# Kernel optimization log

Hardware: AMD Instinct MI355X
Metric: run time of the kernel (lower is better)

## Reference

```python
import jax, jax.numpy as jnp
import numpy as np

NUM_HEADS = 16
NEG = -1e9


def setup_inputs() -> dict:
    key = jax.random.key(0)
    ks = jax.random.split(key, 9)
    B, S, D = 1, 4096, 1024
    s = 1.0 / np.sqrt(D)
    return {
        "x": jax.random.normal(ks[0], (B, S, D), dtype=jnp.float32),
        "wq": jax.random.normal(ks[1], (D, D), dtype=jnp.float32) * s,
        "bq": jax.random.normal(ks[2], (D,), dtype=jnp.float32) * s,
        "wk": jax.random.normal(ks[3], (D, D), dtype=jnp.float32) * s,
        "bk": jax.random.normal(ks[4], (D,), dtype=jnp.float32) * s,
        "wv": jax.random.normal(ks[5], (D, D), dtype=jnp.float32) * s,
        "bv": jax.random.normal(ks[6], (D,), dtype=jnp.float32) * s,
        "wo": jax.random.normal(ks[7], (D, D), dtype=jnp.float32) * s,
        "bo": jax.random.normal(ks[8], (D,), dtype=jnp.float32) * s,
    }


def reference(x, wq, bq, wk, bk, wv, bv, wo, bo):
    B, S, D = x.shape
    H = NUM_HEADS
    hs = D // H
    # torch Linear: y = x @ W^T + b
    q = x @ wq.T + bq
    k = x @ wk.T + bk
    v = x @ wv.T + bv
    # [B, S, D] -> [B, H, S, hs]
    q = q.reshape(B, S, H, hs).transpose(0, 2, 1, 3)
    k = k.reshape(B, S, H, hs).transpose(0, 2, 1, 3)
    v = v.reshape(B, S, H, hs).transpose(0, 2, 1, 3)
    scores = jnp.einsum("bhqd,bhkd->bhqk", q, k) / jnp.sqrt(jnp.asarray(hs, x.dtype))
    causal = jnp.tril(jnp.ones((S, S), dtype=bool))  # True = keep
    scores = jnp.where(causal, scores, jnp.asarray(NEG, x.dtype))
    weights = jax.nn.softmax(scores, axis=-1)
    out = jnp.einsum("bhqk,bhkd->bhqd", weights, v)
    out = out.transpose(0, 2, 1, 3).reshape(B, S, D)
    return out @ wo.T + bo
```

## Files before the change

### kernel.cpp

```cpp
#include <hip/hip_runtime.h>

#define SEQ 4096
#define DM  1024
#define NH  16
#define HS  64

typedef __attribute__((ext_vector_type(8))) _Float16 f16x8;
typedef __attribute__((ext_vector_type(4))) _Float16 f16x4;
typedef __attribute__((ext_vector_type(4))) float    f32x4;

#define MFMA16(a, b, c) __builtin_amdgcn_mfma_f32_16x16x32_f16((a), (b), (c), 0, 0, 0)

#define DPP_ROR_F(x, N) __int_as_float(__builtin_amdgcn_update_dpp( \
    0, __float_as_int(x), 0x120 + (N), 0xF, 0xF, false))

__device__ __forceinline__ float red16_add(float x) {
    x += DPP_ROR_F(x, 1);
    x += DPP_ROR_F(x, 2);
    x += DPP_ROR_F(x, 4);
    x += DPP_ROR_F(x, 8);
    return x;
}

__global__ __launch_bounds__(256) void cast_f32_f16(
    const float* __restrict__ src, _Float16* __restrict__ dst, int n)
{
    int i = (blockIdx.x * 256 + threadIdx.x) * 4;
    if (i < n) {
        float4 v = *reinterpret_cast<const float4*>(src + i);
        f16x4 o = {(_Float16)v.x, (_Float16)v.y, (_Float16)v.z, (_Float16)v.w};
        *reinterpret_cast<f16x4*>(dst + i) = o;
    }
}

__global__ __launch_bounds__(256) void cast4_f32_f16(
    const float* __restrict__ s0, const float* __restrict__ s1,
    const float* __restrict__ s2, const float* __restrict__ s3,
    _Float16* __restrict__ d0, _Float16* __restrict__ d1,
    _Float16* __restrict__ d2, _Float16* __restrict__ d3)
{
    const float* s; _Float16* d;
    switch (blockIdx.y) {
        case 0:  s = s0; d = d0; break;
        case 1:  s = s1; d = d1; break;
        case 2:  s = s2; d = d2; break;
        default: s = s3; d = d3; break;
    }
    int i = (blockIdx.x * 256 + threadIdx.x) * 4;
    float4 v = *reinterpret_cast<const float4*>(s + i);
    f16x4 o = {(_Float16)v.x, (_Float16)v.y, (_Float16)v.z, (_Float16)v.w};
    *reinterpret_cast<f16x4*>(d + i) = o;
}

#define GPAD 72

template <int BIAS_ROW, typename OUT_T>
__global__ __launch_bounds__(256, 2) void gemm_bt_f16(
    const _Float16* __restrict__ A,
    const _Float16* __restrict__ W,
    const float*    __restrict__ bias,
    OUT_T* __restrict__ C,
    int M, int N, int K, float scale)
{
    __shared__ _Float16 As[64][GPAD];
    __shared__ _Float16 Bs[128][GPAD];

    const int t    = threadIdx.x;
    const int w    = t >> 6;
    const int lane = t & 63;
    const int q    = lane >> 4;
    const int l    = lane & 15;
    const int m0   = blockIdx.y * 64;
    const int n0   = blockIdx.x * 128;
    const int wm   = (w & 1) * 32;
    const int wn   = (w >> 1) * 64;

    const int ar = t >> 2, ac = (t & 3) * 16;
    const int br = t >> 1, bc = (t & 1) * 32;
    const _Float16* gA = A + (size_t)(m0 + ar) * K + ac;
    const _Float16* gW = W + (size_t)(n0 + br) * K + bc;

    uint4 ra0 = *reinterpret_cast<const uint4*>(gA);
    uint4 ra1 = *reinterpret_cast<const uint4*>(gA + 8);
    uint4 rb0 = *reinterpret_cast<const uint4*>(gW);
    uint4 rb1 = *reinterpret_cast<const uint4*>(gW + 8);
    uint4 rb2 = *reinterpret_cast<const uint4*>(gW + 16);
    uint4 rb3 = *reinterpret_cast<const uint4*>(gW + 24);

    f32x4 acc[2][4];
    #pragma unroll
    for (int i = 0; i < 2; ++i)
        #pragma unroll
        for (int j = 0; j < 4; ++j) acc[i][j] = (f32x4){0.f, 0.f, 0.f, 0.f};

    for (int k0 = 0; k0 < K; k0 += 64) {
        __syncthreads();
        *reinterpret_cast<uint4*>(&As[ar][ac])      = ra0;
        *reinterpret_cast<uint4*>(&As[ar][ac + 8])  = ra1;
        *reinterpret_cast<uint4*>(&Bs[br][bc])      = rb0;
        *reinterpret_cast<uint4*>(&Bs[br][bc + 8])  = rb1;
        *reinterpret_cast<uint4*>(&Bs[br][bc + 16]) = rb2;
        *reinterpret_cast<uint4*>(&Bs[br][bc + 24]) = rb3;
        if (k0 + 64 < K) {
            ra0 = *reinterpret_cast<const uint4*>(gA + k0 + 64);
            ra1 = *reinterpret_cast<const uint4*>(gA + k0 + 72);
            rb0 = *reinterpret_cast<const uint4*>(gW + k0 + 64);
            rb1 = *reinterpret_cast<const uint4*>(gW + k0 + 72);
            rb2 = *reinterpret_cast<const uint4*>(gW + k0 + 80);
            rb3 = *reinterpret_cast<const uint4*>(gW + k0 + 88);
        }
        __syncthreads();

        #pragma unroll
        for (int ks = 0; ks < 64; ks += 32) {
            f16x8 af[2], bf[4];
            #pragma unroll
            for (int i = 0; i < 2; ++i)
                af[i] = *reinterpret_cast<const f16x8*>(&As[wm + i * 16 + l][ks + q * 8]);
            #pragma unroll
            for (int j = 0; j < 4; ++j)
                bf[j] = *reinterpret_cast<const f16x8*>(&Bs[wn + j * 16 + l][ks + q * 8]);
            #pragma unroll
            for (int i = 0; i < 2; ++i)
                #pragma unroll
                for (int j = 0; j < 4; ++j)
                    acc[i][j] = MFMA16(af[i], bf[j], acc[i][j]);
        }
    }

    #pragma unroll
    for (int i = 0; i < 2; ++i) {
        #pragma unroll
        for (int j = 0; j < 4; ++j) {
            int gnb = n0 + wn + j * 16 + l;
            float bc2 = BIAS_ROW ? 0.f : bias[gnb];
            #pragma unroll
            for (int r = 0; r < 4; ++r) {
                int gm = m0 + wm + i * 16 + q * 4 + r;
                float bb = BIAS_ROW ? bias[gm] : bc2;
                C[(size_t)gm * N + gnb] = (OUT_T)((acc[i][j][r] + bb) * scale);
            }
        }
    }
}

#define APAD 72

__global__ __launch_bounds__(256, 2) void attn_mfma(
    const _Float16* __restrict__ Qg,
    const _Float16* __restrict__ Kg,
    const _Float16* __restrict__ Vt,
    _Float16* __restrict__ O)
{
    __shared__ _Float16 Qs[64][APAD];
    __shared__ _Float16 Ks[64][APAD];
    __shared__ _Float16 Vs[64][APAD];
    __shared__ _Float16 Ps[64][APAD];

    const int t    = threadIdx.x;
    const int h    = blockIdx.x;
    const int bx   = blockIdx.y;
    const int w    = t >> 6;
    const int lane = t & 63;
    const int q    = lane >> 4;
    const int l    = lane & 15;
    const int sr   = t >> 3;
    const int sc   = (t & 7) * 8;

    for (int phase = 0; phase < 2; ++phase) {
        const int qb = phase ? (63 - bx) : bx;

        __syncthreads();
        *reinterpret_cast<uint4*>(&Qs[sr][sc]) =
            *reinterpret_cast<const uint4*>(Qg + (size_t)(qb * 64 + sr) * DM + h * 64 + sc);
        *reinterpret_cast<uint4*>(&Qs[sr + 32][sc]) =
            *reinterpret_cast<const uint4*>(Qg + (size_t)(qb * 64 + sr + 32) * DM + h * 64 + sc);

        uint4 kr0 = *reinterpret_cast<const uint4*>(Kg + (size_t)(sr) * DM + h * 64 + sc);
        uint4 kr1 = *reinterpret_cast<const uint4*>(Kg + (size_t)(sr + 32) * DM + h * 64 + sc);
        uint4 vr0 = *reinterpret_cast<const uint4*>(Vt + (size_t)(h * 64 + sr) * SEQ + sc);
        uint4 vr1 = *reinterpret_cast<const uint4*>(Vt + (size_t)(h * 64 + sr + 32) * SEQ + sc);

        float l_acc[4] = {0.f, 0.f, 0.f, 0.f};
        f32x4 oacc[4];
        #pragma unroll
        for (int nt = 0; nt < 4; ++nt) oacc[nt] = (f32x4){0.f, 0.f, 0.f, 0.f};

        __syncthreads();
        f16x8 aq0 = *reinterpret_cast<const f16x8*>(&Qs[w * 16 + l][q * 8]);
        f16x8 aq1 = *reinterpret_cast<const f16x8*>(&Qs[w * 16 + l][32 + q * 8]);

        const int qrow_base = qb * 64 + w * 16 + q * 4;

        for (int kt = 0; kt <= qb; ++kt) {
            __syncthreads();
            *reinterpret_cast<uint4*>(&Ks[sr][sc])      = kr0;
            *reinterpret_cast<uint4*>(&Ks[sr + 32][sc]) = kr1;
            *reinterpret_cast<uint4*>(&Vs[sr][sc])      = vr0;
            *reinterpret_cast<uint4*>(&Vs[sr + 32][sc]) = vr1;
            if (kt < qb) {
                kr0 = *reinterpret_cast<const uint4*>(
                    Kg + (size_t)((kt + 1) * 64 + sr) * DM + h * 64 + sc);
                kr1 = *reinterpret_cast<const uint4*>(
                    Kg + (size_t)((kt + 1) * 64 + sr + 32) * DM + h * 64 + sc);
                vr0 = *reinterpret_cast<const uint4*>(
                    Vt + (size_t)(h * 64 + sr) * SEQ + (kt + 1) * 64 + sc);
                vr1 = *reinterpret_cast<const uint4*>(
                    Vt + (size_t)(h * 64 + sr + 32) * SEQ + (kt + 1) * 64 + sc);
            }
            __syncthreads();

            f32x4 s[4];
            #pragma unroll
            for (int jt = 0; jt < 4; ++jt) {
                f16x8 bk0 = *reinterpret_cast<const f16x8*>(&Ks[4 * l + jt][q * 8]);
                f16x8 bk1 = *reinterpret_cast<const f16x8*>(&Ks[4 * l + jt][32 + q * 8]);
                f32x4 z = (f32x4){0.f, 0.f, 0.f, 0.f};
                z = MFMA16(aq0, bk0, z);
                z = MFMA16(aq1, bk1, z);
                s[jt] = z;
            }

            const bool diag = (kt == qb);

            #pragma unroll
            for (int r = 0; r < 4; ++r) {
                float p0 = s[0][r], p1 = s[1][r], p2 = s[2][r], p3 = s[3][r];
                if (diag) {
                    const int qg = qrow_base + r;
                    const int kg = kt * 64 + 4 * l;
                    p0 = (kg + 0 <= qg) ? p0 : -1e30f;
                    p1 = (kg + 1 <= qg) ? p1 : -1e30f;
                    p2 = (kg + 2 <= qg) ? p2 : -1e30f;
                    p3 = (kg + 3 <= qg) ? p3 : -1e30f;
                }
                p0 = __builtin_amdgcn_exp2f(p0 - 4.f);
                p1 = __builtin_amdgcn_exp2f(p1 - 4.f);
                p2 = __builtin_amdgcn_exp2f(p2 - 4.f);
                p3 = __builtin_amdgcn_exp2f(p3 - 4.f);
                l_acc[r] += (p0 + p1) + (p2 + p3);
                f16x4 pk = {(_Float16)p0, (_Float16)p1, (_Float16)p2, (_Float16)p3};
                *reinterpret_cast<f16x4*>(&Ps[w * 16 + q * 4 + r][4 * l]) = pk;
            }

            f16x8 ap0 = *reinterpret_cast<const f16x8*>(&Ps[w * 16 + l][q * 8]);
            f16x8 ap1 = *reinterpret_cast<const f16x8*>(&Ps[w * 16 + l][32 + q * 8]);
            #pragma unroll
            for (int nt = 0; nt < 4; ++nt) {
                f16x8 bv0 = *reinterpret_cast<const f16x8*>(&Vs[nt * 16 + l][q * 8]);
                f16x8 bv1 = *reinterpret_cast<const f16x8*>(&Vs[nt * 16 + l][32 + q * 8]);
                oacc[nt] = MFMA16(ap0, bv0, oacc[nt]);
                oacc[nt] = MFMA16(ap1, bv1, oacc[nt]);
            }
        }

        #pragma unroll
        for (int r = 0; r < 4; ++r) {
            float inv = 1.f / red16_add(l_acc[r]);
            size_t row = (size_t)(qb * 64 + w * 16 + q * 4 + r) * DM + h * 64;
            #pragma unroll
            for (int nt = 0; nt < 4; ++nt)
                O[row + nt * 16 + l] = (_Float16)(oacc[nt][r] * inv);
        }
    }
}

extern "C" void kernel_launch(void* const* d_in, const int* in_sizes, int n_in,
                              void* d_out, int out_size, void* d_ws, size_t ws_size,
                              hipStream_t stream)
{
    const float* x  = (const float*)d_in[0];
    const float* wq = (const float*)d_in[1];
    const float* bq = (const float*)d_in[2];
    const float* wk = (const float*)d_in[3];
    const float* bk = (const float*)d_in[4];
    const float* wv = (const float*)d_in[5];
    const float* bv = (const float*)d_in[6];
    const float* wo = (const float*)d_in[7];
    const float* bo = (const float*)d_in[8];
    float* out = (float*)d_out;

    char* ws = (char*)d_ws;
    _Float16* xb  = (_Float16*)(ws);
    _Float16* wqb = (_Float16*)(ws + (8ull  << 20));
    _Float16* wkb = (_Float16*)(ws + (10ull << 20));
    _Float16* wvb = (_Float16*)(ws + (12ull << 20));
    _Float16* wob = (_Float16*)(ws + (14ull << 20));
    _Float16* Qb  = (_Float16*)(ws + (16ull << 20));
    _Float16* Kb  = (_Float16*)(ws + (24ull << 20));
    _Float16* Vtb = (_Float16*)(ws + (32ull << 20));
    _Float16* Ab  = (_Float16*)(ws + (40ull << 20));

    cast_f32_f16<<<dim3(SEQ * DM / 1024), dim3(256), 0, stream>>>(x, xb, SEQ * DM);
    cast4_f32_f16<<<dim3(DM * DM / 1024, 4), dim3(256), 0, stream>>>(
        wq, wk, wv, wo, wqb, wkb, wvb, wob);

    gemm_bt_f16<0, _Float16><<<dim3(DM / 128, SEQ / 64), dim3(256), 0, stream>>>(
        xb, wqb, bq, Qb, SEQ, DM, DM, 0.18033688011112042f);
    gemm_bt_f16<0, _Float16><<<dim3(DM / 128, SEQ / 64), dim3(256), 0, stream>>>(
        xb, wkb, bk, Kb, SEQ, DM, DM, 1.0f);
    gemm_bt_f16<1, _Float16><<<dim3(SEQ / 128, DM / 64), dim3(256), 0, stream>>>(
        wvb, xb, bv, Vtb, DM, SEQ, DM, 1.0f);

    attn_mfma<<<dim3(NH, 32), dim3(256), 0, stream>>>(Qb, Kb, Vtb, Ab);

    gemm_bt_f16<0, float><<<dim3(DM / 128, SEQ / 64), dim3(256), 0, stream>>>(
        Ab, wob, bo, out, SEQ, DM, DM, 1.0f);
}
```

Baseline: 225.4 us.

## Enlarge attention query tile to 128 rows and swap GEMM grid order

The attention kernel now processes 128 query rows per block, with each wave handling two 16-row subtiles. Each K/V tile loaded into shared memory is therefore reused by twice as many queries. Subtiles that lie entirely above the causal diagonal are skipped. The grid is halved to 16x16 blocks, which reduces parallelism and increases register and LDS usage per block. Separately, the GEMM grids are transposed so that blockIdx.x walks M, which changes the order in which tiles are scheduled and how caches are shared between neighbouring blocks.

```diff
diff --git a/kernel.cpp b/kernel.cpp
--- a/kernel.cpp
+++ b/kernel.cpp
@@ -70,8 +70,8 @@
     const int lane = t & 63;
     const int q    = lane >> 4;
     const int l    = lane & 15;
-    const int m0   = blockIdx.y * 64;
-    const int n0   = blockIdx.x * 128;
+    const int m0   = blockIdx.x * 64;
+    const int n0   = blockIdx.y * 128;
     const int wm   = (w & 1) * 32;
     const int wn   = (w >> 1) * 64;
 
@@ -152,10 +152,10 @@
     const _Float16* __restrict__ Vt,
     _Float16* __restrict__ O)
 {
-    __shared__ _Float16 Qs[64][APAD];
+    __shared__ _Float16 Qs[128][APAD];
     __shared__ _Float16 Ks[64][APAD];
     __shared__ _Float16 Vs[64][APAD];
-    __shared__ _Float16 Ps[64][APAD];
+    __shared__ _Float16 Ps[128][APAD];
 
     const int t    = threadIdx.x;
     const int h    = blockIdx.x;
@@ -168,37 +168,47 @@
     const int sc   = (t & 7) * 8;
 
     for (int phase = 0; phase < 2; ++phase) {
-        const int qb = phase ? (63 - bx) : bx;
+        const int qb = phase ? (31 - bx) : bx;
+        const int ktmax = 2 * qb + 1;
 
         __syncthreads();
-        *reinterpret_cast<uint4*>(&Qs[sr][sc]) =
-            *reinterpret_cast<const uint4*>(Qg + (size_t)(qb * 64 + sr) * DM + h * 64 + sc);
-        *reinterpret_cast<uint4*>(&Qs[sr + 32][sc]) =
-            *reinterpret_cast<const uint4*>(Qg + (size_t)(qb * 64 + sr + 32) * DM + h * 64 + sc);
+        #pragma unroll
+        for (int u = 0; u < 4; ++u)
+            *reinterpret_cast<uint4*>(&Qs[sr + u * 32][sc]) =
+                *reinterpret_cast<const uint4*>(
+                    Qg + (size_t)(qb * 128 + sr + u * 32) * DM + h * 64 + sc);
 
         uint4 kr0 = *reinterpret_cast<const uint4*>(Kg + (size_t)(sr) * DM + h * 64 + sc);
         uint4 kr1 = *reinterpret_cast<const uint4*>(Kg + (size_t)(sr + 32) * DM + h * 64 + sc);
         uint4 vr0 = *reinterpret_cast<const uint4*>(Vt + (size_t)(h * 64 + sr) * SEQ + sc);
         uint4 vr1 = *reinterpret_cast<const uint4*>(Vt + (size_t)(h * 64 + sr + 32) * SEQ + sc);
 
-        float l_acc[4] = {0.f, 0.f, 0.f, 0.f};
-        f32x4 oacc[4];
-        #pragma unroll
-        for (int nt = 0; nt < 4; ++nt) oacc[nt] = (f32x4){0.f, 0.f, 0.f, 0.f};
+        float l_acc[2][4] = {};
+        f32x4 oacc[2][4];
+        #pragma unroll
+        for (int i = 0; i < 2; ++i)
+            #pragma unroll
+            for (int nt = 0; nt < 4; ++nt) oacc[i][nt] = (f32x4){0.f, 0.f, 0.f, 0.f};
 
         __syncthreads();
-        f16x8 aq0 = *reinterpret_cast<const f16x8*>(&Qs[w * 16 + l][q * 8]);
-        f16x8 aq1 = *reinterpret_cast<const f16x8*>(&Qs[w * 16 + l][32 + q * 8]);
-
-        const int qrow_base = qb * 64 + w * 16 + q * 4;
-
-        for (int kt = 0; kt <= qb; ++kt) {
+        f16x8 aq[2][2];
+        #pragma unroll
+        for (int i = 0; i < 2; ++i) {
+            aq[i][0] = *reinterpret_cast<const f16x8*>(&Qs[w * 32 + i * 16 + l][q * 8]);
+            aq[i][1] = *reinterpret_cast<const f16x8*>(&Qs[w * 32 + i * 16 + l][32 + q * 8]);
+        }
+
+        const int tfirst0 = qb * 128 + w * 32;
+        const int tlast0  = tfirst0 + 15;
+        const int tlast1  = tfirst0 + 31;
+
+        for (int kt = 0; kt <= ktmax; ++kt) {
             __syncthreads();
             *reinterpret_cast<uint4*>(&Ks[sr][sc])      = kr0;
             *reinterpret_cast<uint4*>(&Ks[sr + 32][sc]) = kr1;
             *reinterpret_cast<uint4*>(&Vs[sr][sc])      = vr0;
             *reinterpret_cast<uint4*>(&Vs[sr + 32][sc]) = vr1;
-            if (kt < qb) {
+            if (kt < ktmax) {
                 kr0 = *reinterpret_cast<const uint4*>(
                     Kg + (size_t)((kt + 1) * 64 + sr) * DM + h * 64 + sc);
                 kr1 = *reinterpret_cast<const uint4*>(
@@ -210,57 +220,81 @@
             }
             __syncthreads();
 
-            f32x4 s[4];
+            if (kt * 64 > tlast1) continue;
+            const bool run0 = (kt * 64 <= tlast0);
+
+            f32x4 s[2][4];
             #pragma unroll
             for (int jt = 0; jt < 4; ++jt) {
                 f16x8 bk0 = *reinterpret_cast<const f16x8*>(&Ks[4 * l + jt][q * 8]);
                 f16x8 bk1 = *reinterpret_cast<const f16x8*>(&Ks[4 * l + jt][32 + q * 8]);
-                f32x4 z = (f32x4){0.f, 0.f, 0.f, 0.f};
-                z = MFMA16(aq0, bk0, z);
-                z = MFMA16(aq1, bk1, z);
-                s[jt] = z;
-            }
-
-            const bool diag = (kt == qb);
-
-            #pragma unroll
-            for (int r = 0; r < 4; ++r) {
-                float p0 = s[0][r], p1 = s[1][r], p2 = s[2][r], p3 = s[3][r];
-                if (diag) {
-                    const int qg = qrow_base + r;
-                    const int kg = kt * 64 + 4 * l;
-                    p0 = (kg + 0 <= qg) ? p0 : -1e30f;
-                    p1 = (kg + 1 <= qg) ? p1 : -1e30f;
-                    p2 = (kg + 2 <= qg) ? p2 : -1e30f;
-                    p3 = (kg + 3 <= qg) ? p3 : -1e30f;
+                #pragma unroll
+                for (int i = 0; i < 2; ++i) {
+                    if (i == 0 && !run0) continue;
+                    f32x4 z = (f32x4){0.f, 0.f, 0.f, 0.f};
+                    z = MFMA16(aq[i][0], bk0, z);
+                    z = MFMA16(aq[i][1], bk1, z);
+                    s[i][jt] = z;
                 }
-                p0 = __builtin_amdgcn_exp2f(p0 - 4.f);
-                p1 = __builtin_amdgcn_exp2f(p1 - 4.f);
-                p2 = __builtin_amdgcn_exp2f(p2 - 4.f);
-                p3 = __builtin_amdgcn_exp2f(p3 - 4.f);
-                l_acc[r] += (p0 + p1) + (p2 + p3);
-                f16x4 pk = {(_Float16)p0, (_Float16)p1, (_Float16)p2, (_Float16)p3};
-                *reinterpret_cast<f16x4*>(&Ps[w * 16 + q * 4 + r][4 * l]) = pk;
-            }
-
-            f16x8 ap0 = *reinterpret_cast<const f16x8*>(&Ps[w * 16 + l][q * 8]);
-            f16x8 ap1 = *reinterpret_cast<const f16x8*>(&Ps[w * 16 + l][32 + q * 8]);
+            }
+
+            #pragma unroll
+            for (int i = 0; i < 2; ++i) {
+                if (i == 0 && !run0) continue;
+                const int tfirst = tfirst0 + i * 16;
+                const bool diag  = (kt * 64 + 63 > tfirst);
+                #pragma unroll
+                for (int r = 0; r < 4; ++r) {
+                    float p0 = s[i][0][r], p1 = s[i][1][r];
+                    float p2 = s[i][2][r], p3 = s[i][3][r];
+                    if (diag) {
+                        const int qg = tfirst + q * 4 + r;
+                        const int kg = kt * 64 + 4 * l;
+                        p0 = (kg + 0 <= qg) ? p0 : -1e30f;
+                        p1 = (kg + 1 <= qg) ? p1 : -1e30f;
+                        p2 = (kg + 2 <= qg) ? p2 : -1e30f;
+                        p3 = (kg + 3 <= qg) ? p3 : -1e30f;
+                    }
+                    p0 = __builtin_amdgcn_exp2f(p0 - 4.f);
+                    p1 = __builtin_amdgcn_exp2f(p1 - 4.f);
+                    p2 = __builtin_amdgcn_exp2f(p2 - 4.f);
+                    p3 = __builtin_amdgcn_exp2f(p3 - 4.f);
+                    l_acc[i][r] += (p0 + p1) + (p2 + p3);
+                    f16x4 pk = {(_Float16)p0, (_Float16)p1, (_Float16)p2, (_Float16)p3};
+                    *reinterpret_cast<f16x4*>(&Ps[w * 32 + i * 16 + q * 4 + r][4 * l]) = pk;
+                }
+            }
+
+            f16x8 ap[2][2];
+            #pragma unroll
+            for (int i = 0; i < 2; ++i) {
+                if (i == 0 && !run0) continue;
+                ap[i][0] = *reinterpret_cast<const f16x8*>(&Ps[w * 32 + i * 16 + l][q * 8]);
+                ap[i][1] = *reinterpret_cast<const f16x8*>(&Ps[w * 32 + i * 16 + l][32 + q * 8]);
+            }
             #pragma unroll
             for (int nt = 0; nt < 4; ++nt) {
                 f16x8 bv0 = *reinterpret_cast<const f16x8*>(&Vs[nt * 16 + l][q * 8]);
                 f16x8 bv1 = *reinterpret_cast<const f16x8*>(&Vs[nt * 16 + l][32 + q * 8]);
-                oacc[nt] = MFMA16(ap0, bv0, oacc[nt]);
-                oacc[nt] = MFMA16(ap1, bv1, oacc[nt]);
-            }
-        }
-
-        #pragma unroll
-        for (int r = 0; r < 4; ++r) {
-            float inv = 1.f / red16_add(l_acc[r]);
-            size_t row = (size_t)(qb * 64 + w * 16 + q * 4 + r) * DM + h * 64;
-            #pragma unroll
-            for (int nt = 0; nt < 4; ++nt)
-                O[row + nt * 16 + l] = (_Float16)(oacc[nt][r] * inv);
+                #pragma unroll
+                for (int i = 0; i < 2; ++i) {
+                    if (i == 0 && !run0) continue;
+                    oacc[i][nt] = MFMA16(ap[i][0], bv0, oacc[i][nt]);
+                    oacc[i][nt] = MFMA16(ap[i][1], bv1, oacc[i][nt]);
+                }
+            }
+        }
+
+        #pragma unroll
+        for (int i = 0; i < 2; ++i) {
+            #pragma unroll
+            for (int r = 0; r < 4; ++r) {
+                float inv = 1.f / red16_add(l_acc[i][r]);
+                size_t row = (size_t)(qb * 128 + w * 32 + i * 16 + q * 4 + r) * DM + h * 64;
+                #pragma unroll
+                for (int nt = 0; nt < 4; ++nt)
+                    O[row + nt * 16 + l] = (_Float16)(oacc[i][nt][r] * inv);
+            }
         }
     }
 }
@@ -295,15 +329,15 @@
     cast4_f32_f16<<<dim3(DM * DM / 1024, 4), dim3(256), 0, stream>>>(
         wq, wk, wv, wo, wqb, wkb, wvb, wob);
 
-    gemm_bt_f16<0, _Float16><<<dim3(DM / 128, SEQ / 64), dim3(256), 0, stream>>>(
+    gemm_bt_f16<0, _Float16><<<dim3(SEQ / 64, DM / 128), dim3(256), 0, stream>>>(
         xb, wqb, bq, Qb, SEQ, DM, DM, 0.18033688011112042f);
-    gemm_bt_f16<0, _Float16><<<dim3(DM / 128, SEQ / 64), dim3(256), 0, stream>>>(
+    gemm_bt_f16<0, _Float16><<<dim3(SEQ / 64, DM / 128), dim3(256), 0, stream>>>(
         xb, wkb, bk, Kb, SEQ, DM, DM, 1.0f);
-    gemm_bt_f16<1, _Float16><<<dim3(SEQ / 128, DM / 64), dim3(256), 0, stream>>>(
+    gemm_bt_f16<1, _Float16><<<dim3(DM / 64, SEQ / 128), dim3(256), 0, stream>>>(
         wvb, xb, bv, Vtb, DM, SEQ, DM, 1.0f);
 
-    attn_mfma<<<dim3(NH, 32), dim3(256), 0, stream>>>(Qb, Kb, Vtb, Ab);
-
-    gemm_bt_f16<0, float><<<dim3(DM / 128, SEQ / 64), dim3(256), 0, stream>>>(
+    attn_mfma<<<dim3(NH, 16), dim3(256), 0, stream>>>(Qb, Kb, Vtb, Ab);
+
+    gemm_bt_f16<0, float><<<dim3(SEQ / 64, DM / 128), dim3(256), 0, stream>>>(
         Ab, wob, bo, out, SEQ, DM, DM, 1.0f);
 }
```

New measurement: 243.7 us. 1.08x slower.
